# Kernel optimization log

Hardware: AMD Instinct MI355X
Metric: run time of the kernel (lower is better)

The kernel has to match this reference:

```python
import jax, jax.numpy as jnp
import numpy as np

N_NODES = 50000

def setup_inputs() -> dict:
    key = jax.random.key(0)
    ks = jax.random.split(key, 4)
    x = jax.random.normal(ks[0], (N_NODES, 64), dtype=jnp.float32)
    edge_index = jax.random.randint(ks[1], (2, 800000), 0, N_NODES, dtype=jnp.int64)
    W1 = jax.random.normal(ks[2], (64, 128), dtype=jnp.float32) * (1.0 / np.sqrt(64))
    b1 = jnp.zeros((128,), dtype=jnp.float32)
    W2 = jax.random.normal(ks[3], (128, 64), dtype=jnp.float32) * (1.0 / np.sqrt(128))
    b2 = jnp.zeros((64,), dtype=jnp.float32)
    eps = jnp.zeros((1,), dtype=jnp.float32)
    return {"x": x, "edge_index": edge_index, "W1": W1, "b1": b1, "W2": W2, "b2": b2, "eps": eps}

def reference(x, edge_index, W1, b1, W2, b2, eps):
    row, col = edge_index[0], edge_index[1]
    # gather neighbor features [E, d] and scatter-add into destination nodes [N, d]
    agg = jax.ops.segment_sum(x[col], row, num_segments=x.shape[0])
    h = (1.0 + eps[0]) * x + agg
    # 2-layer MLP: Linear -> ReLU -> Linear
    h = jax.nn.relu(h @ W1 + b1)
    return h @ W2 + b2
```

## Files before the change

### kernel.cpp

```cpp
#include <hip/hip_runtime.h>

#define N_NODES 50000
#define N_EDGES 800000
#define D 64
#define H 128
#define NLIVE 98
#define NBPAD 128
#define BT 2048
#define NBB 391
#define CAPT 52
#define NT8 49
#define STG 1280
#define SCAP2 352
#define CVB 798

typedef __attribute__((ext_vector_type(8))) short  short8;
typedef __attribute__((ext_vector_type(4))) float  floatx4;
typedef __attribute__((ext_vector_type(4))) unsigned short ushort4v;

__device__ inline unsigned short f2bf(float f) {
    unsigned u = __builtin_bit_cast(unsigned, f);
    u += 0x7FFFu + ((u >> 16) & 1u);
    return (unsigned short)(u >> 16);
}
__device__ inline float bf2f(unsigned short b) {
    unsigned u = (unsigned)b << 16;
    return __builtin_bit_cast(float, u);
}

__global__ __launch_bounds__(1024) void bin_prep(
    const int* __restrict__ row, const int* __restrict__ col,
    int* __restrict__ counts, int* __restrict__ csr,
    int* __restrict__ cursor2,
    const float* __restrict__ x, unsigned short* __restrict__ xb,
    const float* __restrict__ W1, unsigned short* __restrict__ w1t,
    const float* __restrict__ W2, unsigned short* __restrict__ w2t)
{
    int t = threadIdx.x;
    if (blockIdx.x >= NBB) {
        int cb = blockIdx.x - NBB;
        if (cb == 0)
            for (int i = t; i < NLIVE * 32; i += 1024) cursor2[i] = 0;
        int tid = cb * 1024 + t;
        if (tid < 800000) {
            float4 v = ((const float4*)x)[tid];
            ushort4v o;
            o.x = f2bf(v.x); o.y = f2bf(v.y); o.z = f2bf(v.z); o.w = f2bf(v.w);
            ((ushort4v*)xb)[tid] = o;
        } else {
            int i = tid - 800000;
            if (i < D * H) {
                int k = i >> 7, n = i & 127;
                w1t[n * D + k] = f2bf(W1[i]);
            } else if (i < 2 * D * H) {
                int j = i - D * H;
                int k = j >> 6, n = j & 63;
                w2t[n * H + k] = f2bf(W2[j]);
            }
        }
        return;
    }

    __shared__ int cnt[NBPAD];
    __shared__ int loffs[NBPAD];
    __shared__ int sorted[BT];
    __shared__ int wsum[2];

    int lane = t & 63;
    if (t < NBPAD) cnt[t] = 0;
    __syncthreads();

    int base = blockIdx.x * BT;
    int ia = base + t, ib = ia + 1024;
    int ca = min(ia, N_EDGES - 1), cb2 = min(ib, N_EDGES - 1);
    unsigned ra = (unsigned)row[ca], rb = (unsigned)row[cb2];
    unsigned ka = (unsigned)col[ca], kb = (unsigned)col[cb2];
    bool va = ia < N_EDGES, vb = ib < N_EDGES;
    if (va) atomicAdd(&cnt[ra >> 9], 1);
    if (vb) atomicAdd(&cnt[rb >> 9], 1);
    __syncthreads();

    int v = 0, incl = 0;
    if (t < NBPAD) {
        v = cnt[t];
        incl = v;
        #pragma unroll
        for (int d = 1; d < 64; d <<= 1) {
            int y = __shfl_up(incl, d);
            if (lane >= d) incl += y;
        }
        if (lane == 63) wsum[t >> 6] = incl;
    }
    __syncthreads();
    if (t < NBPAD) {
        loffs[t] = incl - v + ((t >= 64) ? wsum[0] : 0);
        if (t < NLIVE) counts[blockIdx.x * NLIVE + t] = min(v, CAPT);
    }
    __syncthreads();

    if (t < NBPAD) cnt[t] = 0;
    __syncthreads();

    if (va) { int b = (int)(ra >> 9); int lp = atomicAdd(&cnt[b], 1);
              sorted[loffs[b] + lp] = (int)((ra << 16) | ka); }
    if (vb) { int b = (int)(rb >> 9); int lp = atomicAdd(&cnt[b], 1);
              sorted[loffs[b] + lp] = (int)((rb << 16) | kb); }
    __syncthreads();

    int nloc = min(BT, N_EDGES - base);
    for (int i = t; i < nloc; i += 1024) {
        unsigned en = (unsigned)sorted[i];
        int b = (int)(en >> 25);
        int rel = i - loffs[b];
        if (rel < CAPT)
            csr[((size_t)blockIdx.x * NLIVE + b) * CAPT + rel] = (int)en;
    }
}

__global__ __launch_bounds__(256, 8) void subsort(
    const int* __restrict__ counts, const int* __restrict__ csr,
    int* __restrict__ cursor2, int* __restrict__ csr2)
{
    __shared__ int tcnt[NT8];
    __shared__ int stage[STG];
    __shared__ int sorted2[STG];
    __shared__ int cnt32[32], loffs[32], gbase[32], curs[32];
    __shared__ int nstage;

    int t = threadIdx.x, lane = t & 63;
    int bucket = blockIdx.x >> 3, q = blockIdx.x & 7;
    int tbeg = q * NT8;
    int ntile = min(NT8, NBB - tbeg);

    if (t < 32) cnt32[t] = 0;
    if (t == 0) nstage = 0;
    if (t < ntile) tcnt[t] = counts[(size_t)(tbeg + t) * NLIVE + bucket];
    __syncthreads();

    for (int s = t; s < ntile * CAPT; s += 256) {
        int tl = s / CAPT, slot = s - tl * CAPT;
        if (slot < tcnt[tl]) {
            int e = csr[((size_t)(tbeg + tl) * NLIVE + bucket) * CAPT + slot];
            int p = atomicAdd(&nstage, 1);
            stage[min(p, STG - 1)] = e;
            atomicAdd(&cnt32[((unsigned)e >> 20) & 31u], 1);
        }
    }
    __syncthreads();

    int nst = min(nstage, STG);
    if (t < 32) {
        int v = cnt32[t];
        int incl = v;
        #pragma unroll
        for (int d = 1; d < 32; d <<= 1) {
            int y = __shfl_up(incl, d);
            if (lane >= d) incl += y;
        }
        loffs[t] = incl - v;
        curs[t]  = incl - v;
        gbase[t] = v ? atomicAdd(&cursor2[bucket * 32 + t], v) : 0;
    }
    __syncthreads();

    for (int i = t; i < nst; i += 256) {
        int e = stage[i];
        int sub = (int)(((unsigned)e >> 20) & 31u);
        int p = atomicAdd(&curs[sub], 1);
        sorted2[min(p, STG - 1)] = e;
    }
    __syncthreads();

    for (int i = t; i < nst; i += 256) {
        unsigned en = (unsigned)sorted2[i];
        int sub = (int)((en >> 20) & 31u);
        int rel = gbase[sub] + (i - loffs[sub]);
        if (rel < SCAP2)
            csr2[((size_t)bucket * 32 + sub) * SCAP2 + rel] =
                (int)(en & 0xFFFFFu);
    }
}

__global__ __launch_bounds__(256, 8) void gather_mlp(
    const float* __restrict__ x, const unsigned short* __restrict__ xb,
    const int* __restrict__ cursor2, const int* __restrict__ csr2,
    const unsigned short* __restrict__ w1t, const float* __restrict__ b1,
    const unsigned short* __restrict__ w2t, const float* __restrict__ b2,
    const float* __restrict__ eps, float* __restrict__ out)
{
    __shared__ int ent[SCAP2];
    __shared__ unsigned short scol[SCAP2];
    __shared__ int cnt16[16], offs[17], curs[16];
    __shared__ unsigned short HB[16][72];
    __shared__ unsigned short HID[16][136];

    int t = threadIdx.x, lane = t & 63, wid = t >> 6;
    int bs = blockIdx.x;
    int bucket = bs >> 5, sub = bs & 31;

    if (t < 16) cnt16[t] = 0;
    __syncthreads();

    int n2 = min(cursor2[bs], SCAP2);
    const int* src = csr2 + (size_t)bs * SCAP2;

    for (int i = t; i < n2; i += 256) {
        int e = src[i];
        ent[i] = e;
        atomicAdd(&cnt16[((unsigned)e >> 16) & 15u], 1);
    }
    __syncthreads();

    if (t < 16) {
        int v = cnt16[t];
        int incl = v;
        #pragma unroll
        for (int d = 1; d < 16; d <<= 1) {
            int y = __shfl_up(incl, d);
            if (lane >= d) incl += y;
        }
        offs[t] = incl - v;
        curs[t] = incl - v;
        if (t == 15) offs[16] = incl;
    }
    __syncthreads();

    for (int i = t; i < n2; i += 256) {
        int e = ent[i];
        int nl = (int)(((unsigned)e >> 16) & 15u);
        int p = atomicAdd(&curs[nl], 1);
        scol[p] = (unsigned short)(e & 0xFFFF);
    }
    __syncthreads();

    float ep = 1.0f + eps[0];
    int half = lane >> 5, fl = lane & 31;
    #pragma unroll 1
    for (int nn = 0; nn < 4; ++nn) {
        int nl = wid * 4 + nn;
        int node = bucket * 512 + sub * 16 + nl;
        int jb = offs[nl], je = offs[nl + 1];
        float s0a = 0.f, s1a = 0.f, s0b = 0.f, s1b = 0.f;
        float s0c = 0.f, s1c = 0.f, s0d = 0.f, s1d = 0.f;
        int j = jb;
        for (; j + 8 <= je; j += 8) {
            int c0 = scol[j + half];
            int c1 = scol[j + 2 + half];
            int c2 = scol[j + 4 + half];
            int c3 = scol[j + 6 + half];
            ushort2 p0 = *(const ushort2*)&xb[c0 * D + 2 * fl];
            ushort2 p1 = *(const ushort2*)&xb[c1 * D + 2 * fl];
            ushort2 p2 = *(const ushort2*)&xb[c2 * D + 2 * fl];
            ushort2 p3 = *(const ushort2*)&xb[c3 * D + 2 * fl];
            s0a += bf2f(p0.x); s1a += bf2f(p0.y);
            s0b += bf2f(p1.x); s1b += bf2f(p1.y);
            s0c += bf2f(p2.x); s1c += bf2f(p2.y);
            s0d += bf2f(p3.x); s1d += bf2f(p3.y);
        }
        for (; j < je; j += 2) {
            if (j + half < je) {
                int c = scol[j + half];
                ushort2 p = *(const ushort2*)&xb[c * D + 2 * fl];
                s0a += bf2f(p.x); s1a += bf2f(p.y);
            }
        }
        float s0 = (s0a + s0b) + (s0c + s0d);
        float s1 = (s1a + s1b) + (s1c + s1d);
        s0 += __shfl_xor(s0, 32);
        s1 += __shfl_xor(s1, 32);
        if (half == 0) {
            float2 xv = {0.f, 0.f};
            if (node < N_NODES) xv = *(const float2*)&x[(size_t)node * D + 2 * fl];
            ushort2 o;
            o.x = f2bf(fmaf(ep, xv.x, s0));
            o.y = f2bf(fmaf(ep, xv.y, s1));
            *(ushort2*)&HB[nl][2 * fl] = o;
        }
    }
    __syncthreads();

    if (wid == 0) {
        int m = lane & 15, q = lane >> 4;
        short8 a0 = *(const short8*)&HB[m][q * 8];
        short8 a1 = *(const short8*)&HB[m][32 + q * 8];

        #pragma unroll
        for (int nt = 0; nt < 8; ++nt) {
            float bias = b1[nt * 16 + m];
            floatx4 acc = {bias, bias, bias, bias};
            short8 w0 = *(const short8*)&w1t[(nt * 16 + m) * D + q * 8];
            short8 w1 = *(const short8*)&w1t[(nt * 16 + m) * D + 32 + q * 8];
            acc = __builtin_amdgcn_mfma_f32_16x16x32_bf16(a0, w0, acc, 0, 0, 0);
            acc = __builtin_amdgcn_mfma_f32_16x16x32_bf16(a1, w1, acc, 0, 0, 0);
            #pragma unroll
            for (int r = 0; r < 4; ++r) {
                float hv = fmaxf(acc[r], 0.0f);
                HID[q * 4 + r][nt * 16 + m] = f2bf(hv);
            }
        }

        short8 ha[4];
        #pragma unroll
        for (int kc2 = 0; kc2 < 4; ++kc2)
            ha[kc2] = *(const short8*)&HID[m][kc2 * 32 + q * 8];

        #pragma unroll
        for (int nt2 = 0; nt2 < 4; ++nt2) {
            float bias = b2[nt2 * 16 + m];
            floatx4 acc = {bias, bias, bias, bias};
            #pragma unroll
            for (int kc2 = 0; kc2 < 4; ++kc2) {
                short8 w = *(const short8*)&w2t[(nt2 * 16 + m) * H + kc2 * 32 + q * 8];
                acc = __builtin_amdgcn_mfma_f32_16x16x32_bf16(ha[kc2], w, acc, 0, 0, 0);
            }
            #pragma unroll
            for (int r = 0; r < 4; ++r) {
                int nn2 = bucket * 512 + sub * 16 + q * 4 + r;
                if (nn2 < N_NODES) out[(size_t)nn2 * D + nt2 * 16 + m] = acc[r];
            }
        }
    }
}

extern "C" void kernel_launch(void* const* d_in, const int* in_sizes, int n_in,
                              void* d_out, int out_size, void* d_ws, size_t ws_size,
                              hipStream_t stream) {
    const float* x   = (const float*)d_in[0];
    const int*   ei  = (const int*)  d_in[1];
    const float* W1  = (const float*)d_in[2];
    const float* b1  = (const float*)d_in[3];
    const float* W2  = (const float*)d_in[4];
    const float* b2  = (const float*)d_in[5];
    const float* eps = (const float*)d_in[6];
    float* out = (float*)d_out;

    unsigned short* xb  = (unsigned short*)d_ws;
    unsigned short* w1t = xb + (size_t)N_NODES * D;
    unsigned short* w2t = w1t + D * H;
    int* csr     = (int*)(w2t + D * H);
    int* counts  = csr + (size_t)NBB * NLIVE * CAPT;
    int* csr2    = counts + (size_t)NBB * NLIVE;
    int* cursor2 = csr2 + (size_t)NLIVE * 32 * SCAP2;

    const int* row = ei;
    const int* col = ei + N_EDGES;

    bin_prep<<<NBB + CVB, 1024, 0, stream>>>(row, col, counts, csr, cursor2,
                                             x, xb, W1, w1t, W2, w2t);
    subsort<<<NLIVE * 8, 256, 0, stream>>>(counts, csr, cursor2, csr2);
    gather_mlp<<<NLIVE * 32, 256, 0, stream>>>(x, xb, cursor2, csr2,
                                               w1t, b1, w2t, b2, eps, out);
}
```

Measured before the change: 121.6 us.

## Fuse subsort into gather-MLP kernel, each block filtering its 64-node slice from bucket tiles

Drops the separate subsort pass and its csr2/cursor2 global buffers. Each 512-thread block now scans every tile's CSR chunk for its bucket, keeps only edges whose destination falls in its 64-node eighth, sorts them in LDS, then gathers and runs the MLP across four MFMA waves. The counts array is transposed so a bucket's counts are contiguous. This saves one launch and a global round trip, but each block reads the whole bucket (8x redundant reads of csr), and the larger LDS footprint may reduce occupancy.

```diff
diff --git a/kernel.cpp b/kernel.cpp
--- a/kernel.cpp
+++ b/kernel.cpp
@@ -9,9 +9,7 @@
 #define BT 2048
 #define NBB 391
 #define CAPT 52
-#define NT8 49
-#define STG 1280
-#define SCAP2 352
+#define STG 1408
 #define CVB 798
 
 typedef __attribute__((ext_vector_type(8))) short  short8;
@@ -31,17 +29,13 @@
 __global__ __launch_bounds__(1024) void bin_prep(
     const int* __restrict__ row, const int* __restrict__ col,
     int* __restrict__ counts, int* __restrict__ csr,
-    int* __restrict__ cursor2,
     const float* __restrict__ x, unsigned short* __restrict__ xb,
     const float* __restrict__ W1, unsigned short* __restrict__ w1t,
     const float* __restrict__ W2, unsigned short* __restrict__ w2t)
 {
     int t = threadIdx.x;
     if (blockIdx.x >= NBB) {
-        int cb = blockIdx.x - NBB;
-        if (cb == 0)
-            for (int i = t; i < NLIVE * 32; i += 1024) cursor2[i] = 0;
-        int tid = cb * 1024 + t;
+        int tid = (blockIdx.x - NBB) * 1024 + t;
         if (tid < 800000) {
             float4 v = ((const float4*)x)[tid];
             ushort4v o;
@@ -94,7 +88,7 @@
     __syncthreads();
     if (t < NBPAD) {
         loffs[t] = incl - v + ((t >= 64) ? wsum[0] : 0);
-        if (t < NLIVE) counts[blockIdx.x * NLIVE + t] = min(v, CAPT);
+        if (t < NLIVE) counts[(size_t)t * NBB + blockIdx.x] = min(v, CAPT);
     }
     __syncthreads();
 
@@ -117,129 +111,73 @@
     }
 }
 
-__global__ __launch_bounds__(256, 8) void subsort(
+__global__ __launch_bounds__(512, 8) void sub_gather_mlp(
+    const float* __restrict__ x, const unsigned short* __restrict__ xb,
     const int* __restrict__ counts, const int* __restrict__ csr,
-    int* __restrict__ cursor2, int* __restrict__ csr2)
-{
-    __shared__ int tcnt[NT8];
-    __shared__ int stage[STG];
-    __shared__ int sorted2[STG];
-    __shared__ int cnt32[32], loffs[32], gbase[32], curs[32];
-    __shared__ int nstage;
-
-    int t = threadIdx.x, lane = t & 63;
-    int bucket = blockIdx.x >> 3, q = blockIdx.x & 7;
-    int tbeg = q * NT8;
-    int ntile = min(NT8, NBB - tbeg);
-
-    if (t < 32) cnt32[t] = 0;
-    if (t == 0) nstage = 0;
-    if (t < ntile) tcnt[t] = counts[(size_t)(tbeg + t) * NLIVE + bucket];
-    __syncthreads();
-
-    for (int s = t; s < ntile * CAPT; s += 256) {
-        int tl = s / CAPT, slot = s - tl * CAPT;
-        if (slot < tcnt[tl]) {
-            int e = csr[((size_t)(tbeg + tl) * NLIVE + bucket) * CAPT + slot];
-            int p = atomicAdd(&nstage, 1);
-            stage[min(p, STG - 1)] = e;
-            atomicAdd(&cnt32[((unsigned)e >> 20) & 31u], 1);
-        }
-    }
-    __syncthreads();
-
-    int nst = min(nstage, STG);
-    if (t < 32) {
-        int v = cnt32[t];
-        int incl = v;
-        #pragma unroll
-        for (int d = 1; d < 32; d <<= 1) {
-            int y = __shfl_up(incl, d);
-            if (lane >= d) incl += y;
-        }
-        loffs[t] = incl - v;
-        curs[t]  = incl - v;
-        gbase[t] = v ? atomicAdd(&cursor2[bucket * 32 + t], v) : 0;
-    }
-    __syncthreads();
-
-    for (int i = t; i < nst; i += 256) {
-        int e = stage[i];
-        int sub = (int)(((unsigned)e >> 20) & 31u);
-        int p = atomicAdd(&curs[sub], 1);
-        sorted2[min(p, STG - 1)] = e;
-    }
-    __syncthreads();
-
-    for (int i = t; i < nst; i += 256) {
-        unsigned en = (unsigned)sorted2[i];
-        int sub = (int)((en >> 20) & 31u);
-        int rel = gbase[sub] + (i - loffs[sub]);
-        if (rel < SCAP2)
-            csr2[((size_t)bucket * 32 + sub) * SCAP2 + rel] =
-                (int)(en & 0xFFFFFu);
-    }
-}
-
-__global__ __launch_bounds__(256, 8) void gather_mlp(
-    const float* __restrict__ x, const unsigned short* __restrict__ xb,
-    const int* __restrict__ cursor2, const int* __restrict__ csr2,
     const unsigned short* __restrict__ w1t, const float* __restrict__ b1,
     const unsigned short* __restrict__ w2t, const float* __restrict__ b2,
     const float* __restrict__ eps, float* __restrict__ out)
 {
-    __shared__ int ent[SCAP2];
-    __shared__ unsigned short scol[SCAP2];
-    __shared__ int cnt16[16], offs[17], curs[16];
-    __shared__ unsigned short HB[16][72];
-    __shared__ unsigned short HID[16][136];
+    __shared__ int tcnt[NBB];
+    __shared__ int stage[STG];
+    __shared__ unsigned short scol[STG];
+    __shared__ int cnt64[64], offs[65], curs[64];
+    __shared__ int nstage;
+    __shared__ unsigned short HB[64][72];
+    __shared__ unsigned short HID[4][16][136];
 
     int t = threadIdx.x, lane = t & 63, wid = t >> 6;
-    int bs = blockIdx.x;
-    int bucket = bs >> 5, sub = bs & 31;
-
-    if (t < 16) cnt16[t] = 0;
-    __syncthreads();
-
-    int n2 = min(cursor2[bs], SCAP2);
-    const int* src = csr2 + (size_t)bs * SCAP2;
-
-    for (int i = t; i < n2; i += 256) {
-        int e = src[i];
-        ent[i] = e;
-        atomicAdd(&cnt16[((unsigned)e >> 16) & 15u], 1);
-    }
-    __syncthreads();
-
-    if (t < 16) {
-        int v = cnt16[t];
+    int bucket = blockIdx.x >> 3, eighth = blockIdx.x & 7;
+
+    if (t < 64) cnt64[t] = 0;
+    if (t == 0) nstage = 0;
+    for (int i = t; i < NBB; i += 512) tcnt[i] = counts[(size_t)bucket * NBB + i];
+    __syncthreads();
+
+    for (int s = t; s < NBB * CAPT; s += 512) {
+        int tl = s / CAPT, slot = s - tl * CAPT;
+        if (slot < tcnt[tl]) {
+            int e = csr[((size_t)tl * NLIVE + bucket) * CAPT + slot];
+            int loc9 = (int)(((unsigned)e >> 16) & 511u);
+            if ((loc9 >> 6) == eighth) {
+                int p = atomicAdd(&nstage, 1);
+                if (p < STG) stage[p] = e;
+                atomicAdd(&cnt64[loc9 & 63], 1);
+            }
+        }
+    }
+    __syncthreads();
+
+    if (t < 64) {
+        int v = cnt64[t];
         int incl = v;
         #pragma unroll
-        for (int d = 1; d < 16; d <<= 1) {
+        for (int d = 1; d < 64; d <<= 1) {
             int y = __shfl_up(incl, d);
             if (lane >= d) incl += y;
         }
         offs[t] = incl - v;
         curs[t] = incl - v;
-        if (t == 15) offs[16] = incl;
-    }
-    __syncthreads();
-
-    for (int i = t; i < n2; i += 256) {
-        int e = ent[i];
-        int nl = (int)(((unsigned)e >> 16) & 15u);
+        if (t == 63) offs[64] = incl;
+    }
+    __syncthreads();
+
+    int nst = min(nstage, STG);
+    for (int i = t; i < nst; i += 512) {
+        int e = stage[i];
+        int nl = (int)(((unsigned)e >> 16) & 63u);
         int p = atomicAdd(&curs[nl], 1);
-        scol[p] = (unsigned short)(e & 0xFFFF);
+        if (p < STG) scol[p] = (unsigned short)(e & 0xFFFF);
     }
     __syncthreads();
 
     float ep = 1.0f + eps[0];
     int half = lane >> 5, fl = lane & 31;
     #pragma unroll 1
-    for (int nn = 0; nn < 4; ++nn) {
-        int nl = wid * 4 + nn;
-        int node = bucket * 512 + sub * 16 + nl;
-        int jb = offs[nl], je = offs[nl + 1];
+    for (int nn = 0; nn < 8; ++nn) {
+        int nl = wid * 8 + nn;
+        int node = bucket * 512 + eighth * 64 + nl;
+        int jb = min(offs[nl], STG), je = min(offs[nl + 1], STG);
         float s0a = 0.f, s1a = 0.f, s0b = 0.f, s1b = 0.f;
         float s0c = 0.f, s1c = 0.f, s0d = 0.f, s1d = 0.f;
         int j = jb;
@@ -279,10 +217,10 @@
     }
     __syncthreads();
 
-    if (wid == 0) {
+    if (wid < 4) {
         int m = lane & 15, q = lane >> 4;
-        short8 a0 = *(const short8*)&HB[m][q * 8];
-        short8 a1 = *(const short8*)&HB[m][32 + q * 8];
+        short8 a0 = *(const short8*)&HB[wid * 16 + m][q * 8];
+        short8 a1 = *(const short8*)&HB[wid * 16 + m][32 + q * 8];
 
         #pragma unroll
         for (int nt = 0; nt < 8; ++nt) {
@@ -295,14 +233,14 @@
             #pragma unroll
             for (int r = 0; r < 4; ++r) {
                 float hv = fmaxf(acc[r], 0.0f);
-                HID[q * 4 + r][nt * 16 + m] = f2bf(hv);
+                HID[wid][q * 4 + r][nt * 16 + m] = f2bf(hv);
             }
         }
 
         short8 ha[4];
         #pragma unroll
         for (int kc2 = 0; kc2 < 4; ++kc2)
-            ha[kc2] = *(const short8*)&HID[m][kc2 * 32 + q * 8];
+            ha[kc2] = *(const short8*)&HID[wid][m][kc2 * 32 + q * 8];
 
         #pragma unroll
         for (int nt2 = 0; nt2 < 4; ++nt2) {
@@ -315,7 +253,7 @@
             }
             #pragma unroll
             for (int r = 0; r < 4; ++r) {
-                int nn2 = bucket * 512 + sub * 16 + q * 4 + r;
+                int nn2 = bucket * 512 + eighth * 64 + wid * 16 + q * 4 + r;
                 if (nn2 < N_NODES) out[(size_t)nn2 * D + nt2 * 16 + m] = acc[r];
             }
         }
@@ -337,17 +275,14 @@
     unsigned short* xb  = (unsigned short*)d_ws;
     unsigned short* w1t = xb + (size_t)N_NODES * D;
     unsigned short* w2t = w1t + D * H;
-    int* csr     = (int*)(w2t + D * H);
-    int* counts  = csr + (size_t)NBB * NLIVE * CAPT;
-    int* csr2    = counts + (size_t)NBB * NLIVE;
-    int* cursor2 = csr2 + (size_t)NLIVE * 32 * SCAP2;
+    int* csr    = (int*)(w2t + D * H);
+    int* counts = csr + (size_t)NBB * NLIVE * CAPT;
 
     const int* row = ei;
     const int* col = ei + N_EDGES;
 
-    bin_prep<<<NBB + CVB, 1024, 0, stream>>>(row, col, counts, csr, cursor2,
+    bin_prep<<<NBB + CVB, 1024, 0, stream>>>(row, col, counts, csr,
                                              x, xb, W1, w1t, W2, w2t);
-    subsort<<<NLIVE * 8, 256, 0, stream>>>(counts, csr, cursor2, csr2);
-    gather_mlp<<<NLIVE * 32, 256, 0, stream>>>(x, xb, cursor2, csr2,
-                                               w1t, b1, w2t, b2, eps, out);
-}
+    sub_gather_mlp<<<NLIVE * 8, 512, 0, stream>>>(x, xb, counts, csr,
+                                                  w1t, b1, w2t, b2, eps, out);
+}
```

Measured after the change: 136.0 us. 1.12x slower.
